# Performance work log

Hardware: AMD Instinct MI355X
Metric: run time of the kernel (lower is better)

The kernel has to match this reference:

```python
import jax, jax.numpy as jnp
import numpy as np

B, T, D, P = 32, 512, 256, 8
MEL_MAX = T * (P - 1)  # 3584, worst-case expanded length


def setup_inputs() -> dict:
    key = jax.random.key(0)
    k0, k1, k2 = jax.random.split(key, 3)
    x = jax.random.normal(k0, (B, T, D), dtype=jnp.float32)
    # Xavier-uniform-ish scaled weights
    W1 = jax.random.normal(k1, (D, D), dtype=jnp.float32) * (1.0 / np.sqrt(D))
    b1 = jnp.zeros((D,), dtype=jnp.float32)
    W2 = jax.random.normal(k2, (P, D), dtype=jnp.float32) * (1.0 / np.sqrt(D))
    b2 = jnp.zeros((P,), dtype=jnp.float32)
    return {"x": x, "W1": W1, "b1": b1, "W2": W2, "b2": b2,
            "mel_max_length": MEL_MAX}


def reference(x, W1, b1, W2, b2, mel_max_length):
    # DurationPredictor: Linear -> ReLU -> Linear -> softmax
    h = jax.nn.relu(jnp.einsum('btd,ed->bte', x, W1) + b1)
    P_probs = jax.nn.softmax(jnp.einsum('btd,pd->btp', h, W2) + b2, axis=-1)
    # transfer (eval): duration = argmax over class dim
    dur = jnp.argmax(P_probs, axis=-1)  # [B,T] ints in [0, P-1]; alpha=1.0
    # Vectorized LR/expand: frame t maps to the token whose cumulative
    # duration interval contains t.
    cs = jnp.cumsum(dur, axis=1)                 # [B,T] inclusive cumsum
    total = cs[:, -1]                            # [B] mel lengths
    t = jnp.arange(mel_max_length)               # [M]
    src = jax.vmap(lambda c: jnp.searchsorted(c, t, side='right'))(cs)  # [B,M]
    src = jnp.minimum(src, x.shape[1] - 1)
    out = jnp.take_along_axis(x, src[..., None], axis=1)  # [B,M,D]
    mask = (t[None, :] < total[:, None])[..., None]       # pad beyond length
    return jnp.where(mask, out, jnp.zeros((), dtype=x.dtype))
```

## Files before the change

kernel.cpp:

```cpp
#include <hip/hip_runtime.h>

#define B_ 32
#define T_ 512
#define D_ 256
#define P_ 8
#define BT (B_*T_)
#define KT 32
#define NKT (D_/KT)
#define RPW 8
#define RPB 32

typedef float f4 __attribute__((ext_vector_type(4)));

__global__ void k_transpose(const float* __restrict__ W1, float* __restrict__ w1t) {
  int d = blockIdx.x;
  int e = threadIdx.x;
  w1t[d * D_ + e] = W1[e * D_ + d];
}

__global__ __launch_bounds__(256, 2) void k_dur(
    const float* __restrict__ x, const float* __restrict__ w1t,
    const float* __restrict__ b1, const float* __restrict__ W2,
    const float* __restrict__ b2, int* __restrict__ dur)
{
  __shared__ float wst[2][KT][D_];
  __shared__ float xst[2][RPB][KT];

  const int tid  = threadIdx.x;
  const int lane = tid & 63;
  const int wave = tid >> 6;
  const int row0 = blockIdx.x * RPB;

  auto stage = [&](int kt, int buf) {
    {
      const float* g = x + (size_t)(row0 + wave * 8 + (lane >> 3)) * D_
                         + kt * KT + (lane & 7) * 4;
      __builtin_amdgcn_global_load_lds(
          (const __attribute__((address_space(1))) void*)g,
          (__attribute__((address_space(3))) void*)&xst[buf][wave * 8][0], 16, 0, 0);
    }
    for (int i = 0; i < 8; ++i) {
      int dd = wave * 8 + i;
      const float* g = w1t + (size_t)(kt * KT + dd) * D_ + lane * 4;
      __builtin_amdgcn_global_load_lds(
          (const __attribute__((address_space(1))) void*)g,
          (__attribute__((address_space(3))) void*)&wst[buf][dd][0], 16, 0, 0);
    }
  };

  stage(0, 0);
  __syncthreads();

  f4 b1v = *(const f4*)(b1 + lane * 4);
  f4 acc[RPW];
  #pragma unroll
  for (int i = 0; i < RPW; ++i) acc[i] = b1v;

  for (int kt = 0; kt < NKT; ++kt) {
    const int cur = kt & 1;
    if (kt + 1 < NKT) stage(kt + 1, cur ^ 1);

    f4 loc[RPW];
    #pragma unroll
    for (int i = 0; i < RPW; ++i) loc[i] = (f4){0.f, 0.f, 0.f, 0.f};

    #pragma unroll
    for (int dq = 0; dq < KT / 4; ++dq) {
      f4 wv[4];
      #pragma unroll
      for (int j = 0; j < 4; ++j) wv[j] = *(const f4*)&wst[cur][dq * 4 + j][lane * 4];
      #pragma unroll
      for (int i = 0; i < RPW; ++i) {
        f4 xv = *(const f4*)&xst[cur][wave * 8 + i][dq * 4];
        loc[i] += xv.x * wv[0];
        loc[i] += xv.y * wv[1];
        loc[i] += xv.z * wv[2];
        loc[i] += xv.w * wv[3];
      }
    }
    #pragma unroll
    for (int i = 0; i < RPW; ++i) acc[i] += loc[i];

    __syncthreads();
  }

  #pragma unroll
  for (int i = 0; i < RPW; ++i)
    #pragma unroll
    for (int c = 0; c < 4; ++c) acc[i][c] = fmaxf(acc[i][c], 0.f);

  f4 w2r[P_];
  #pragma unroll
  for (int p = 0; p < P_; ++p) w2r[p] = *(const f4*)(W2 + p * D_ + lane * 4);
  float b2r[P_];
  #pragma unroll
  for (int p = 0; p < P_; ++p) b2r[p] = b2[p];

  float v[64];
  #pragma unroll
  for (int r = 0; r < 8; ++r)
    #pragma unroll
    for (int p = 0; p < P_; ++p) {
      f4 h = acc[r];
      v[r * 8 + p] = h[0]*w2r[p][0] + h[1]*w2r[p][1] + h[2]*w2r[p][2] + h[3]*w2r[p][3];
    }

  #pragma unroll
  for (int step = 0; step < 3; ++step) {
    const int s = 1 << step;
    const int hl = 32 >> step;
    const bool upper = (lane & s) != 0;
    #pragma unroll
    for (int i = 0; i < hl; ++i) {
      float a = v[i], b = v[i + hl];
      float send = upper ? a : b;
      float recv = __shfl_xor(send, s, 64);
      v[i] = (upper ? b : a) + recv;
    }
  }
  #pragma unroll
  for (int s = 8; s < 64; s <<= 1)
    #pragma unroll
    for (int i = 0; i < 8; ++i) v[i] += __shfl_xor(v[i], s, 64);

  if (lane < 8) {
    float best = v[0] + b2r[0];
    int am = 0;
    #pragma unroll
    for (int p = 1; p < P_; ++p) {
      float L = v[p] + b2r[p];
      if (L > best) { best = L; am = p; }
    }
    int r = ((lane & 1) << 2) | (lane & 2) | ((lane & 4) >> 2);
    dur[row0 + wave * 8 + r] = am;
  }
}

__global__ void k_scan(const int* __restrict__ dur, int* __restrict__ src, int mel) {
  __shared__ int wsum[8];
  int t = threadIdx.x, b = blockIdx.x;
  int lane = t & 63, wave = t >> 6;
  int d = dur[b * T_ + t];
  int v = d;
  #pragma unroll
  for (int s = 1; s < 64; s <<= 1) {
    int u = __shfl_up(v, s, 64);
    if (lane >= s) v += u;
  }
  if (lane == 63) wsum[wave] = v;
  __syncthreads();
  if (t == 0) {
    int run = 0;
    #pragma unroll
    for (int i = 0; i < 8; ++i) { run += wsum[i]; wsum[i] = run; }
  }
  __syncthreads();
  int cs = v + (wave ? wsum[wave - 1] : 0);
  int start = cs - d;
  int total = wsum[7];
  for (int m = start; m < cs; ++m) src[b * mel + m] = t;
  for (int m = total + t; m < mel; m += T_) src[b * mel + m] = -1;
}

__global__ __launch_bounds__(256) void k_gather(
    const float* __restrict__ x, const int* __restrict__ src,
    float* __restrict__ out, int mel)
{
  int lane = threadIdx.x & 63;
  int wave = threadIdx.x >> 6;
  int m = blockIdx.x * 4 + wave;
  int b = blockIdx.y;
  if (m >= mel) return;
  int s = src[b * mel + m];
  f4 val = {0.f, 0.f, 0.f, 0.f};
  if (s >= 0) val = *(const f4*)(x + ((size_t)b * T_ + s) * D_ + lane * 4);
  *(f4*)(out + ((size_t)b * mel + m) * D_ + lane * 4) = val;
}

extern "C" void kernel_launch(void* const* d_in, const int* in_sizes, int n_in,
                              void* d_out, int out_size, void* d_ws, size_t ws_size,
                              hipStream_t stream) {
  const float* x  = (const float*)d_in[0];
  const float* W1 = (const float*)d_in[1];
  const float* b1 = (const float*)d_in[2];
  const float* W2 = (const float*)d_in[3];
  const float* b2 = (const float*)d_in[4];
  float* out = (float*)d_out;

  int mel = out_size / (B_ * D_);

  float* w1t = (float*)d_ws;
  int*   dur = (int*)((char*)d_ws + D_ * D_ * sizeof(float));
  int*   src = dur + BT;

  k_transpose<<<D_, D_, 0, stream>>>(W1, w1t);
  k_dur<<<BT / RPB, 256, 0, stream>>>(x, w1t, b1, W2, b2, dur);
  k_scan<<<B_, T_, 0, stream>>>(dur, src, mel);
  k_gather<<<dim3((mel + 3) / 4, B_), 256, 0, stream>>>(x, src, out, mel);
}
```

Baseline: 65.11 us.

## Compute duration logits with bf16 MFMA and recheck near-tie rows in fp32

Replaces the fp32 FMA GEMM in the duration predictor with bf16 MFMA 16x16x32 instructions. W1 is converted to bf16 once and x is converted on the fly. Rows whose top-two logits differ by less than a fixed margin are collected through an atomic counter and recomputed exactly in fp32 by a new fix-up kernel, so the argmax still matches. This adds an extra launch and an atomic path, and correctness depends on the margin being large enough to cover bf16 error.

```diff
diff --git a/kernel.cpp b/kernel.cpp
--- a/kernel.cpp
+++ b/kernel.cpp
@@ -5,134 +5,196 @@
 #define D_ 256
 #define P_ 8
 #define BT (B_*T_)
-#define KT 32
-#define NKT (D_/KT)
-#define RPW 8
-#define RPB 32
+#define EPS 0.08f
 
 typedef float f4 __attribute__((ext_vector_type(4)));
-
-__global__ void k_transpose(const float* __restrict__ W1, float* __restrict__ w1t) {
-  int d = blockIdx.x;
-  int e = threadIdx.x;
-  w1t[d * D_ + e] = W1[e * D_ + d];
-}
-
-__global__ __launch_bounds__(256, 2) void k_dur(
-    const float* __restrict__ x, const float* __restrict__ w1t,
+typedef __attribute__((ext_vector_type(8))) short short8;
+
+__device__ inline unsigned short f2bf(float f) {
+  unsigned u = __builtin_bit_cast(unsigned, f);
+  u += 0x7fffu + ((u >> 16) & 1u);
+  return (unsigned short)(u >> 16);
+}
+
+__global__ void k_prep(const float* __restrict__ W1, unsigned short* __restrict__ W1b,
+                       int* __restrict__ cnt) {
+  int i = blockIdx.x * 256 + threadIdx.x;
+  W1b[i] = f2bf(W1[i]);
+  if (i == 0) *cnt = 0;
+}
+
+__global__ __launch_bounds__(256) void k_dur(
+    const float* __restrict__ x, const unsigned short* __restrict__ W1b,
     const float* __restrict__ b1, const float* __restrict__ W2,
-    const float* __restrict__ b2, int* __restrict__ dur)
+    const float* __restrict__ b2, int* __restrict__ dur,
+    int* __restrict__ cnt, int* __restrict__ flagged)
 {
-  __shared__ float wst[2][KT][D_];
-  __shared__ float xst[2][RPB][KT];
-
-  const int tid  = threadIdx.x;
-  const int lane = tid & 63;
-  const int wave = tid >> 6;
-  const int row0 = blockIdx.x * RPB;
-
-  auto stage = [&](int kt, int buf) {
+  __shared__ float lp[4][32][P_];
+
+  const int tid = threadIdx.x;
+  const int l   = tid & 63;
+  const int w   = tid >> 6;
+  const int row0 = blockIdx.x * 32;
+  const int n0  = w * 64;
+  const int l15 = l & 15, lk = l >> 4;
+
+  f4 acc[2][4] = {};
+
+  #pragma unroll
+  for (int ks = 0; ks < 8; ++ks) {
+    short8 bf[4];
+    #pragma unroll
+    for (int nt = 0; nt < 4; ++nt)
+      bf[nt] = *(const short8*)(W1b + (size_t)(n0 + nt * 16 + l15) * D_ + ks * 32 + lk * 8);
+    short8 af[2];
+    #pragma unroll
+    for (int mt = 0; mt < 2; ++mt) {
+      const float* ap = x + (size_t)(row0 + mt * 16 + l15) * D_ + ks * 32 + lk * 8;
+      f4 lo = *(const f4*)ap, hi = *(const f4*)(ap + 4);
+      short8 t;
+      t[0] = (short)f2bf(lo[0]); t[1] = (short)f2bf(lo[1]);
+      t[2] = (short)f2bf(lo[2]); t[3] = (short)f2bf(lo[3]);
+      t[4] = (short)f2bf(hi[0]); t[5] = (short)f2bf(hi[1]);
+      t[6] = (short)f2bf(hi[2]); t[7] = (short)f2bf(hi[3]);
+      af[mt] = t;
+    }
+    #pragma unroll
+    for (int mt = 0; mt < 2; ++mt)
+      #pragma unroll
+      for (int nt = 0; nt < 4; ++nt)
+        acc[mt][nt] = __builtin_amdgcn_mfma_f32_16x16x32_bf16(af[mt], bf[nt], acc[mt][nt], 0, 0, 0);
+  }
+
+  float b1v[4], w2v[4][P_];
+  #pragma unroll
+  for (int nt = 0; nt < 4; ++nt) {
+    int e = n0 + nt * 16 + l15;
+    b1v[nt] = b1[e];
+    #pragma unroll
+    for (int p = 0; p < P_; ++p) w2v[nt][p] = W2[p * D_ + e];
+  }
+
+  #pragma unroll
+  for (int mt = 0; mt < 2; ++mt) {
+    float pl[4][P_];
+    #pragma unroll
+    for (int r = 0; r < 4; ++r)
+      #pragma unroll
+      for (int p = 0; p < P_; ++p) pl[r][p] = 0.f;
+
+    #pragma unroll
+    for (int nt = 0; nt < 4; ++nt)
+      #pragma unroll
+      for (int r = 0; r < 4; ++r) {
+        float h = fmaxf(acc[mt][nt][r] + b1v[nt], 0.f);
+        #pragma unroll
+        for (int p = 0; p < P_; ++p) pl[r][p] = fmaf(h, w2v[nt][p], pl[r][p]);
+      }
+    #pragma unroll
+    for (int s = 1; s < 16; s <<= 1)
+      #pragma unroll
+      for (int r = 0; r < 4; ++r)
+        #pragma unroll
+        for (int p = 0; p < P_; ++p) pl[r][p] += __shfl_xor(pl[r][p], s, 64);
+
+    if (l15 == 0)
+      #pragma unroll
+      for (int r = 0; r < 4; ++r)
+        #pragma unroll
+        for (int p = 0; p < P_; ++p) lp[w][mt * 16 + lk * 4 + r][p] = pl[r][p];
+  }
+  __syncthreads();
+
+  {
+    int row = tid >> 3, p = tid & 7;
+    float top = b2[p] + lp[0][row][p] + lp[1][row][p] + lp[2][row][p] + lp[3][row][p];
+    int   tp  = p;
+    float sec = -__builtin_inff();
+    #pragma unroll
+    for (int s = 1; s < 8; s <<= 1) {
+      float ov = __shfl_xor(top, s, 64);
+      int   op = __shfl_xor(tp,  s, 64);
+      float os = __shfl_xor(sec, s, 64);
+      bool take = (ov > top) || (ov == top && op < tp);
+      float loser = take ? top : ov;
+      top = take ? ov : top;
+      tp  = take ? op : tp;
+      sec = fmaxf(loser, fmaxf(sec, os));
+    }
+    if ((tid & 7) == 0) {
+      dur[row0 + row] = tp;
+      if (top - sec < EPS) {
+        int i = atomicAdd(cnt, 1);
+        flagged[i] = row0 + row;
+      }
+    }
+  }
+}
+
+__global__ __launch_bounds__(256) void k_fix(
+    const float* __restrict__ x, const float* __restrict__ W1,
+    const float* __restrict__ b1, const float* __restrict__ W2,
+    const float* __restrict__ b2, int* __restrict__ dur,
+    const int* __restrict__ cnt, const int* __restrict__ flagged)
+{
+  __shared__ int   ridx[8];
+  __shared__ float xs[8][D_];
+  __shared__ float hs[8][D_];
+  const int t = threadIdx.x;
+  const int n = *cnt;
+
+  for (int base = blockIdx.x * 8; base < n; base += 128 * 8) {
+    if (t < 8 && base + t < n) ridx[t] = flagged[base + t];
+    __syncthreads();
     {
-      const float* g = x + (size_t)(row0 + wave * 8 + (lane >> 3)) * D_
-                         + kt * KT + (lane & 7) * 4;
-      __builtin_amdgcn_global_load_lds(
-          (const __attribute__((address_space(1))) void*)g,
-          (__attribute__((address_space(3))) void*)&xst[buf][wave * 8][0], 16, 0, 0);
-    }
-    for (int i = 0; i < 8; ++i) {
-      int dd = wave * 8 + i;
-      const float* g = w1t + (size_t)(kt * KT + dd) * D_ + lane * 4;
-      __builtin_amdgcn_global_load_lds(
-          (const __attribute__((address_space(1))) void*)g,
-          (__attribute__((address_space(3))) void*)&wst[buf][dd][0], 16, 0, 0);
-    }
-  };
-
-  stage(0, 0);
-  __syncthreads();
-
-  f4 b1v = *(const f4*)(b1 + lane * 4);
-  f4 acc[RPW];
-  #pragma unroll
-  for (int i = 0; i < RPW; ++i) acc[i] = b1v;
-
-  for (int kt = 0; kt < NKT; ++kt) {
-    const int cur = kt & 1;
-    if (kt + 1 < NKT) stage(kt + 1, cur ^ 1);
-
-    f4 loc[RPW];
-    #pragma unroll
-    for (int i = 0; i < RPW; ++i) loc[i] = (f4){0.f, 0.f, 0.f, 0.f};
-
-    #pragma unroll
-    for (int dq = 0; dq < KT / 4; ++dq) {
-      f4 wv[4];
-      #pragma unroll
-      for (int j = 0; j < 4; ++j) wv[j] = *(const f4*)&wst[cur][dq * 4 + j][lane * 4];
-      #pragma unroll
-      for (int i = 0; i < RPW; ++i) {
-        f4 xv = *(const f4*)&xst[cur][wave * 8 + i][dq * 4];
-        loc[i] += xv.x * wv[0];
-        loc[i] += xv.y * wv[1];
-        loc[i] += xv.z * wv[2];
-        loc[i] += xv.w * wv[3];
-      }
-    }
-    #pragma unroll
-    for (int i = 0; i < RPW; ++i) acc[i] += loc[i];
-
-    __syncthreads();
-  }
-
-  #pragma unroll
-  for (int i = 0; i < RPW; ++i)
-    #pragma unroll
-    for (int c = 0; c < 4; ++c) acc[i][c] = fmaxf(acc[i][c], 0.f);
-
-  f4 w2r[P_];
-  #pragma unroll
-  for (int p = 0; p < P_; ++p) w2r[p] = *(const f4*)(W2 + p * D_ + lane * 4);
-  float b2r[P_];
-  #pragma unroll
-  for (int p = 0; p < P_; ++p) b2r[p] = b2[p];
-
-  float v[64];
-  #pragma unroll
-  for (int r = 0; r < 8; ++r)
-    #pragma unroll
-    for (int p = 0; p < P_; ++p) {
-      f4 h = acc[r];
-      v[r * 8 + p] = h[0]*w2r[p][0] + h[1]*w2r[p][1] + h[2]*w2r[p][2] + h[3]*w2r[p][3];
-    }
-
-  #pragma unroll
-  for (int step = 0; step < 3; ++step) {
-    const int s = 1 << step;
-    const int hl = 32 >> step;
-    const bool upper = (lane & s) != 0;
-    #pragma unroll
-    for (int i = 0; i < hl; ++i) {
-      float a = v[i], b = v[i + hl];
-      float send = upper ? a : b;
-      float recv = __shfl_xor(send, s, 64);
-      v[i] = (upper ? b : a) + recv;
-    }
-  }
-  #pragma unroll
-  for (int s = 8; s < 64; s <<= 1)
-    #pragma unroll
-    for (int i = 0; i < 8; ++i) v[i] += __shfl_xor(v[i], s, 64);
-
-  if (lane < 8) {
-    float best = v[0] + b2r[0];
-    int am = 0;
-    #pragma unroll
-    for (int p = 1; p < P_; ++p) {
-      float L = v[p] + b2r[p];
-      if (L > best) { best = L; am = p; }
-    }
-    int r = ((lane & 1) << 2) | (lane & 2) | ((lane & 4) >> 2);
-    dur[row0 + wave * 8 + r] = am;
+      int j = t >> 5, c = (t & 31) * 8;
+      if (base + j < n) {
+        const float* p = x + (size_t)ridx[j] * D_ + c;
+        f4 a = *(const f4*)p, b = *(const f4*)(p + 4);
+        *(f4*)&xs[j][c] = a; *(f4*)&xs[j][c + 4] = b;
+      }
+    }
+    __syncthreads();
+
+    {
+      int e = t;
+      float ar[8];
+      #pragma unroll
+      for (int r = 0; r < 8; ++r) ar[r] = b1[e];
+      for (int kt = 0; kt < 8; ++kt) {
+        float wreg[32];
+        #pragma unroll
+        for (int q = 0; q < 8; ++q)
+          *(f4*)&wreg[q * 4] = *(const f4*)(W1 + (size_t)e * D_ + kt * 32 + q * 4);
+        #pragma unroll
+        for (int r = 0; r < 8; ++r) {
+          float lo = 0.f;
+          #pragma unroll
+          for (int d = 0; d < 32; ++d) lo = fmaf(xs[r][kt * 32 + d], wreg[d], lo);
+          ar[r] += lo;
+        }
+      }
+      #pragma unroll
+      for (int r = 0; r < 8; ++r) hs[r][e] = fmaxf(ar[r], 0.f);
+    }
+    __syncthreads();
+
+    if (t < 64) {
+      int r = t >> 3, p = t & 7;
+      float lo = b2[p];
+      for (int e = 0; e < D_; ++e) lo = fmaf(hs[r][e], W2[p * D_ + e], lo);
+      float top = lo; int tp = p;
+      #pragma unroll
+      for (int s = 1; s < 8; s <<= 1) {
+        float ov = __shfl_xor(top, s, 64);
+        int   op = __shfl_xor(tp,  s, 64);
+        bool take = (ov > top) || (ov == top && op < tp);
+        top = take ? ov : top;
+        tp  = take ? op : tp;
+      }
+      if ((t & 7) == 0 && base + r < n) dur[ridx[r]] = tp;
+    }
+    __syncthreads();
   }
 }
 
@@ -189,12 +251,16 @@
 
   int mel = out_size / (B_ * D_);
 
-  float* w1t = (float*)d_ws;
-  int*   dur = (int*)((char*)d_ws + D_ * D_ * sizeof(float));
-  int*   src = dur + BT;
-
-  k_transpose<<<D_, D_, 0, stream>>>(W1, w1t);
-  k_dur<<<BT / RPB, 256, 0, stream>>>(x, w1t, b1, W2, b2, dur);
+  char* wp = (char*)d_ws;
+  unsigned short* W1b = (unsigned short*)wp;          wp += D_ * D_ * sizeof(short);
+  int* cnt     = (int*)wp;                            wp += 64;
+  int* flagged = (int*)wp;                            wp += BT * sizeof(int);
+  int* dur     = (int*)wp;                            wp += BT * sizeof(int);
+  int* src     = (int*)wp;
+
+  k_prep<<<D_ * D_ / 256, 256, 0, stream>>>(W1, W1b, cnt);
+  k_dur<<<BT / 32, 256, 0, stream>>>(x, W1b, b1, W2, b2, dur, cnt, flagged);
+  k_fix<<<128, 256, 0, stream>>>(x, W1, b1, W2, b2, dur, cnt, flagged);
   k_scan<<<B_, T_, 0, stream>>>(dur, src, mel);
   k_gather<<<dim3((mel + 3) / 4, B_), 256, 0, stream>>>(x, src, out, mel);
 }
```

New measurement: 119.6 us. 83.7% more time.
